# Optimization experiments

Hardware: AMD Instinct MI355X
Metric: run time of the kernel (lower is better)

Reference implementation:

```python
import jax, jax.numpy as jnp
import numpy as np

N_NODES = 100000
N_EDGES = 3200000
D_IN = 128
D_OUT = 128


def setup_inputs() -> dict:
    key = jax.random.key(0)
    k1, k2, k3 = jax.random.split(key, 3)
    x = jax.random.normal(k1, (N_NODES, D_IN), dtype=jnp.float32)
    edge_index = jax.random.randint(k2, (2, N_EDGES), 0, N_NODES, dtype=jnp.int64)
    # Glorot-style init for the GCN linear weight [out, in]
    weight = jax.random.normal(k3, (D_OUT, D_IN), dtype=jnp.float32) * (1.0 / np.sqrt(D_IN))
    bias = jnp.zeros((D_OUT,), dtype=jnp.float32)
    return {"x": x, "edge_index": edge_index, "weight": weight, "bias": bias}


def reference(x, edge_index, weight, bias):
    """LinearEncoder.forward: (GCNConv(x, edge_index), 0).

    GCNConv: out = D^-1/2 (A + I) D^-1/2 (x W^T) + b  (symmetric norm, self-loops).
    """
    n = x.shape[0]
    src = edge_index[0]
    dst = edge_index[1]
    # add self-loops
    loops = jnp.arange(n, dtype=src.dtype)
    src = jnp.concatenate([src, loops])
    dst = jnp.concatenate([dst, loops])
    # degree (in-degree over destination nodes, unit edge weights)
    ones = jnp.ones(src.shape[0], dtype=x.dtype)
    deg = jax.ops.segment_sum(ones, dst, num_segments=n)
    deg_inv_sqrt = jnp.where(deg > 0, jax.lax.rsqrt(deg), 0.0).astype(x.dtype)
    norm = deg_inv_sqrt[src] * deg_inv_sqrt[dst]  # [E+N]
    # dense transform first (as in PyG GCNConv), then sparse aggregation
    h = x @ weight.T  # [N, D_OUT]
    msgs = h[src] * norm[:, None]  # [E+N, D_OUT]
    out = jax.ops.segment_sum(msgs, dst, num_segments=n) + bias
    return (out, 0)
```

## Files before the change

kernel.cpp:

```cpp
#include <hip/hip_runtime.h>
#include <hip/hip_bf16.h>

#define N_NODES 100000
#define N_EDGES 3200000
#define D 128

typedef unsigned short u16;

#define BKT_W 512
#define NBKT 196
#define NSH 8
#define CAPS 2304
#define CAPB (NSH * CAPS)
#define EPB 6400
#define P1B 500
#define EPT 25

#define CY_BLOCKS 6250
#define CW_BLOCKS 8

typedef __attribute__((ext_vector_type(8))) short bf16x8;
typedef __attribute__((ext_vector_type(4))) float f32x4;

__device__ __forceinline__ float bf2f(u16 u) {
    union { unsigned i; float f; } a; a.i = ((unsigned)u) << 16; return a.f;
}
__device__ __forceinline__ u16 f2bf(float f) {
    __hip_bfloat16 b = __float2bfloat16(f);
    return *(u16*)&b;
}

__global__ __launch_bounds__(256) void p1_multisplit(const int* __restrict__ ei,
                                                     int* __restrict__ bcnt,
                                                     unsigned* __restrict__ bbuf) {
    __shared__ unsigned s1[EPB];
    __shared__ unsigned s2[EPB];
    __shared__ int hist[NBKT], lbase[NBKT], cur[NBKT], gbase[NBKT];
    __shared__ int sc[256];
    int t = threadIdx.x, blk = blockIdx.x;
    int sh = blk & (NSH - 1);
    int e0 = blk * EPB;
    if (t < NBKT) hist[t] = 0;
    __syncthreads();

    unsigned char bk[EPT];
#pragma unroll
    for (int k = 0; k < EPT; ++k) {
        int i = k * 256 + t;
        int s = ei[e0 + i];
        int d = ei[N_EDGES + e0 + i];
        unsigned bkt = (unsigned)d >> 9;
        bk[k] = (unsigned char)bkt;
        s1[i] = ((unsigned)s << 9) | ((unsigned)d & 511u);
        atomicAdd(&hist[bkt], 1);
    }
    __syncthreads();

    if (t < NBKT) gbase[t] = atomicAdd(&bcnt[t * NSH + sh], hist[t]);

    sc[t] = (t < NBKT) ? hist[t] : 0;
    __syncthreads();
    for (int o = 1; o < 256; o <<= 1) {
        int u = (t >= o) ? sc[t - o] : 0;
        __syncthreads();
        sc[t] += u;
        __syncthreads();
    }
    if (t < NBKT) { int ex = sc[t] - hist[t]; lbase[t] = ex; cur[t] = ex; }
    __syncthreads();

#pragma unroll
    for (int k = 0; k < EPT; ++k) {
        int i = k * 256 + t;
        int p = atomicAdd(&cur[bk[k]], 1);
        s2[p] = s1[i];
    }
    __syncthreads();

    int wave = t >> 6, lane = t & 63;
    for (int bkt = wave; bkt < NBKT; bkt += 4) {
        int n = hist[bkt], lb = lbase[bkt], gb = gbase[bkt];
        unsigned* dst = bbuf + ((size_t)bkt * NSH + sh) * CAPS;
        for (int j = lane; j < n; j += 64) {
            int p = gb + j;
            if (p < CAPS) dst[p] = s2[lb + j];
        }
    }
}

__global__ __launch_bounds__(256) void p2_localsort(const unsigned* __restrict__ bbuf,
                                                    const int* __restrict__ bcnt,
                                                    int* __restrict__ sorted,
                                                    int* __restrict__ beg_g,
                                                    int* __restrict__ cnt_g,
                                                    float* __restrict__ dinv_g) {
    __shared__ int hist[BKT_W], cur[BKT_W], shcnt[NSH];
    __shared__ int sc[256];
    int b = blockIdx.x, t = threadIdx.x;
    if (t < NSH) { int m = bcnt[b * NSH + t]; shcnt[t] = m > CAPS ? CAPS : m; }
    hist[t] = 0; hist[t + 256] = 0;
    __syncthreads();

    for (int sh = 0; sh < NSH; ++sh) {
        int m = shcnt[sh];
        const unsigned* p = bbuf + ((size_t)b * NSH + sh) * CAPS;
        for (int i = t; i < m; i += 256) atomicAdd(&hist[p[i] & 511u], 1);
    }
    __syncthreads();

    int a0 = hist[2 * t], a1 = hist[2 * t + 1];
    sc[t] = a0 + a1;
    __syncthreads();
    for (int o = 1; o < 256; o <<= 1) {
        int u = (t >= o) ? sc[t - o] : 0;
        __syncthreads();
        sc[t] += u;
        __syncthreads();
    }
    int exp_ = sc[t] - a0 - a1;
    cur[2 * t] = exp_;
    cur[2 * t + 1] = exp_ + a0;
    __syncthreads();

#pragma unroll
    for (int q = 0; q < 2; ++q) {
        int l = t + q * 256;
        int node = b * BKT_W + l;
        if (node < N_NODES) {
            int c = hist[l];
            cnt_g[node] = c;
            beg_g[node] = b * CAPB + cur[l];
            dinv_g[node] = rsqrtf((float)(c + 1));
        }
    }
    __syncthreads();

    int* dst = sorted + (size_t)b * CAPB;
    for (int sh = 0; sh < NSH; ++sh) {
        int m = shcnt[sh];
        const unsigned* p = bbuf + ((size_t)b * NSH + sh) * CAPS;
        for (int i = t; i < m; i += 256) {
            unsigned w = p[i];
            int pp = atomicAdd(&cur[w & 511u], 1);
            dst[pp] = (int)(w >> 9);
        }
    }
}

__global__ __launch_bounds__(256) void convert_yw(const float* __restrict__ x,
                                                  const float* __restrict__ dinv,
                                                  const float* __restrict__ w,
                                                  u16* __restrict__ y,
                                                  u16* __restrict__ wbf) {
    int blk = blockIdx.x;
    if (blk < CY_BLOCKS) {
        int gid = blk * 256 + threadIdx.x;
        size_t e = (size_t)gid * 8;
        float dn = dinv[gid >> 4];
        const float4* xp = (const float4*)(x + e);
        float4 a = xp[0], b = xp[1];
        union { u16 h[8]; uint4 v; } o;
        o.h[0] = f2bf(a.x * dn); o.h[1] = f2bf(a.y * dn);
        o.h[2] = f2bf(a.z * dn); o.h[3] = f2bf(a.w * dn);
        o.h[4] = f2bf(b.x * dn); o.h[5] = f2bf(b.y * dn);
        o.h[6] = f2bf(b.z * dn); o.h[7] = f2bf(b.w * dn);
        ((uint4*)y)[gid] = o.v;
    } else {
        int idx = (blk - CY_BLOCKS) * 256 + threadIdx.x;
        const float4* wp = (const float4*)(w + (size_t)idx * 8);
        float4 a = wp[0], b = wp[1];
        union { u16 h[8]; uint4 v; } o;
        o.h[0] = f2bf(a.x); o.h[1] = f2bf(a.y);
        o.h[2] = f2bf(a.z); o.h[3] = f2bf(a.w);
        o.h[4] = f2bf(b.x); o.h[5] = f2bf(b.y);
        o.h[6] = f2bf(b.z); o.h[7] = f2bf(b.w);
        ((uint4*)wbf)[idx] = o.v;
    }
}

__global__ void aggregate_y_kernel(const u16* __restrict__ y, const float* __restrict__ dinv,
                                   const int* __restrict__ beg_g, const int* __restrict__ cnt_g,
                                   const int* __restrict__ sorted_src,
                                   float* __restrict__ agg) {
    int n = blockIdx.x;
    int t = threadIdx.x;
    float acc = bf2f(y[(size_t)n * D + t]);
    int c = cnt_g[n];
    int beg = beg_g[n];
    int i = 0;
    for (; i + 8 <= c; i += 8) {
        int s[8];
#pragma unroll
        for (int j = 0; j < 8; ++j) s[j] = sorted_src[beg + i + j];
        float v[8];
#pragma unroll
        for (int j = 0; j < 8; ++j) v[j] = bf2f(y[(size_t)s[j] * D + t]);
#pragma unroll
        for (int j = 0; j < 8; ++j) acc += v[j];
    }
    for (; i + 4 <= c; i += 4) {
        int s0 = sorted_src[beg + i];
        int s1 = sorted_src[beg + i + 1];
        int s2 = sorted_src[beg + i + 2];
        int s3 = sorted_src[beg + i + 3];
        float v0 = bf2f(y[(size_t)s0 * D + t]);
        float v1 = bf2f(y[(size_t)s1 * D + t]);
        float v2 = bf2f(y[(size_t)s2 * D + t]);
        float v3 = bf2f(y[(size_t)s3 * D + t]);
        acc += v0; acc += v1; acc += v2; acc += v3;
    }
    for (; i < c; ++i) {
        int s = sorted_src[beg + i];
        acc += bf2f(y[(size_t)s * D + t]);
    }
    agg[(size_t)n * D + t] = acc * dinv[n];
}

__global__ __launch_bounds__(256) void gemm_mfma(const u16* __restrict__ wbf,
                                                 const float* __restrict__ bias,
                                                 float* __restrict__ out) {
    int t = threadIdx.x;
    int wave = t >> 6, lane = t & 63;
    int n0 = blockIdx.x * 64 + wave * 16;
    int lrow = lane & 15;
    int quad = lane >> 4;

    int arow = n0 + lrow;
    const float* ap = out + (size_t)(arow < N_NODES ? arow : 0) * D;
    bf16x8 afrag[4];
#pragma unroll
    for (int kt = 0; kt < 4; ++kt) {
        int k0 = kt * 32 + quad * 8;
        f32x4 x0 = *(const f32x4*)(ap + k0);
        f32x4 x1 = *(const f32x4*)(ap + k0 + 4);
        bf16x8 a;
        a[0] = (short)f2bf(x0.x); a[1] = (short)f2bf(x0.y);
        a[2] = (short)f2bf(x0.z); a[3] = (short)f2bf(x0.w);
        a[4] = (short)f2bf(x1.x); a[5] = (short)f2bf(x1.y);
        a[6] = (short)f2bf(x1.z); a[7] = (short)f2bf(x1.w);
        afrag[kt] = a;
    }

#pragma unroll
    for (int jt = 0; jt < 8; ++jt) {
        int j0 = jt * 16;
        f32x4 acc = {0.f, 0.f, 0.f, 0.f};
#pragma unroll
        for (int kt = 0; kt < 4; ++kt) {
            int k0 = kt * 32 + quad * 8;
            bf16x8 b = *(const bf16x8*)(wbf + (size_t)(j0 + lrow) * D + k0);
            acc = __builtin_amdgcn_mfma_f32_16x16x32_bf16(afrag[kt], b, acc, 0, 0, 0);
        }
        float bb = bias[j0 + lrow];
#pragma unroll
        for (int i = 0; i < 4; ++i) {
            int n = n0 + quad * 4 + i;
            if (n < N_NODES) out[(size_t)n * D + j0 + lrow] = acc[i] + bb;
        }
    }
    if (blockIdx.x == 0 && t == 0) out[(size_t)N_NODES * D] = 0.f;
}

extern "C" void kernel_launch(void* const* d_in, const int* in_sizes, int n_in,
                              void* d_out, int out_size, void* d_ws, size_t ws_size,
                              hipStream_t stream) {
    const float* x = (const float*)d_in[0];
    const int* ei = (const int*)d_in[1];
    const float* w = (const float*)d_in[2];
    const float* bias = (const float*)d_in[3];
    float* out = (float*)d_out;

    char* ws = (char*)d_ws;
    size_t o = 0;
    auto alloc = [&](size_t bytes) -> char* {
        char* p = ws + o;
        o = (o + bytes + 511) & ~(size_t)511;
        return p;
    };
    char* regionA = alloc((size_t)N_NODES * D * 2);
    unsigned* bbuf = (unsigned*)regionA;
    u16* y = (u16*)regionA;
    int* sorted = (int*)alloc((size_t)NBKT * CAPB * 4);
    int* cnt = (int*)alloc((size_t)N_NODES * 4);
    int* beg = (int*)alloc((size_t)N_NODES * 4);
    float* dinv = (float*)alloc((size_t)N_NODES * 4);
    int* bcnt = (int*)alloc((size_t)NBKT * NSH * 4);
    u16* wbf = (u16*)alloc((size_t)D * D * 2);

    hipMemsetAsync(bcnt, 0, (size_t)NBKT * NSH * 4, stream);

    p1_multisplit<<<P1B, 256, 0, stream>>>(ei, bcnt, bbuf);
    p2_localsort<<<NBKT, 256, 0, stream>>>(bbuf, bcnt, sorted, beg, cnt, dinv);
    convert_yw<<<CY_BLOCKS + CW_BLOCKS, 256, 0, stream>>>(x, dinv, w, y, wbf);
    aggregate_y_kernel<<<N_NODES, 128, 0, stream>>>(y, dinv, beg, cnt, sorted, out);
    gemm_mfma<<<(N_NODES + 63) / 64, 256, 0, stream>>>(wbf, bias, out);
}
```

Baseline: 349.2 us.

## Transform before aggregation: fuse x conversion into GEMM, wave-per-node aggregation

Reorders the pipeline so the GEMM reads fp32 x directly, scales rows by dinv and writes bf16 h. The sparse aggregation then sums h and applies dinv and bias in its epilogue. This removes the separate x-to-bf16 conversion pass and the fp32 aggregate write/readback that the final GEMM used to do. The weight conversion moves into extra blocks of the local-sort kernel. Aggregation now gives each node one wave, with each lane reading two packed bf16 values as one 32-bit load and a 16-wide unrolled gather. Aggregating after the transform changes where bf16 rounding happens, which may slightly change numerics.

```diff
diff --git a/kernel.cpp b/kernel.cpp
--- a/kernel.cpp
+++ b/kernel.cpp
@@ -16,7 +16,6 @@
 #define P1B 500
 #define EPT 25
 
-#define CY_BLOCKS 6250
 #define CW_BLOCKS 8
 
 typedef __attribute__((ext_vector_type(8))) short bf16x8;
@@ -24,6 +23,9 @@
 
 __device__ __forceinline__ float bf2f(u16 u) {
     union { unsigned i; float f; } a; a.i = ((unsigned)u) << 16; return a.f;
+}
+__device__ __forceinline__ float asf(unsigned u) {
+    union { unsigned i; float f; } a; a.i = u; return a.f;
 }
 __device__ __forceinline__ u16 f2bf(float f) {
     __hip_bfloat16 b = __float2bfloat16(f);
@@ -93,10 +95,26 @@
                                                     int* __restrict__ sorted,
                                                     int* __restrict__ beg_g,
                                                     int* __restrict__ cnt_g,
-                                                    float* __restrict__ dinv_g) {
+                                                    float* __restrict__ dinv_g,
+                                                    const float* __restrict__ w,
+                                                    u16* __restrict__ wbf) {
     __shared__ int hist[BKT_W], cur[BKT_W], shcnt[NSH];
     __shared__ int sc[256];
     int b = blockIdx.x, t = threadIdx.x;
+
+    if (b >= NBKT) {
+        int idx = (b - NBKT) * 256 + t;
+        const float4* wp = (const float4*)(w + (size_t)idx * 8);
+        float4 a = wp[0], bb = wp[1];
+        union { u16 h[8]; uint4 v; } o;
+        o.h[0] = f2bf(a.x); o.h[1] = f2bf(a.y);
+        o.h[2] = f2bf(a.z); o.h[3] = f2bf(a.w);
+        o.h[4] = f2bf(bb.x); o.h[5] = f2bf(bb.y);
+        o.h[6] = f2bf(bb.z); o.h[7] = f2bf(bb.w);
+        ((uint4*)wbf)[idx] = o.v;
+        return;
+    }
+
     if (t < NSH) { int m = bcnt[b * NSH + t]; shcnt[t] = m > CAPS ? CAPS : m; }
     hist[t] = 0; hist[t + 256] = 0;
     __syncthreads();
@@ -140,85 +158,17 @@
         int m = shcnt[sh];
         const unsigned* p = bbuf + ((size_t)b * NSH + sh) * CAPS;
         for (int i = t; i < m; i += 256) {
-            unsigned w = p[i];
-            int pp = atomicAdd(&cur[w & 511u], 1);
-            dst[pp] = (int)(w >> 9);
-        }
-    }
-}
-
-__global__ __launch_bounds__(256) void convert_yw(const float* __restrict__ x,
-                                                  const float* __restrict__ dinv,
-                                                  const float* __restrict__ w,
-                                                  u16* __restrict__ y,
-                                                  u16* __restrict__ wbf) {
-    int blk = blockIdx.x;
-    if (blk < CY_BLOCKS) {
-        int gid = blk * 256 + threadIdx.x;
-        size_t e = (size_t)gid * 8;
-        float dn = dinv[gid >> 4];
-        const float4* xp = (const float4*)(x + e);
-        float4 a = xp[0], b = xp[1];
-        union { u16 h[8]; uint4 v; } o;
-        o.h[0] = f2bf(a.x * dn); o.h[1] = f2bf(a.y * dn);
-        o.h[2] = f2bf(a.z * dn); o.h[3] = f2bf(a.w * dn);
-        o.h[4] = f2bf(b.x * dn); o.h[5] = f2bf(b.y * dn);
-        o.h[6] = f2bf(b.z * dn); o.h[7] = f2bf(b.w * dn);
-        ((uint4*)y)[gid] = o.v;
-    } else {
-        int idx = (blk - CY_BLOCKS) * 256 + threadIdx.x;
-        const float4* wp = (const float4*)(w + (size_t)idx * 8);
-        float4 a = wp[0], b = wp[1];
-        union { u16 h[8]; uint4 v; } o;
-        o.h[0] = f2bf(a.x); o.h[1] = f2bf(a.y);
-        o.h[2] = f2bf(a.z); o.h[3] = f2bf(a.w);
-        o.h[4] = f2bf(b.x); o.h[5] = f2bf(b.y);
-        o.h[6] = f2bf(b.z); o.h[7] = f2bf(b.w);
-        ((uint4*)wbf)[idx] = o.v;
-    }
-}
-
-__global__ void aggregate_y_kernel(const u16* __restrict__ y, const float* __restrict__ dinv,
-                                   const int* __restrict__ beg_g, const int* __restrict__ cnt_g,
-                                   const int* __restrict__ sorted_src,
-                                   float* __restrict__ agg) {
-    int n = blockIdx.x;
-    int t = threadIdx.x;
-    float acc = bf2f(y[(size_t)n * D + t]);
-    int c = cnt_g[n];
-    int beg = beg_g[n];
-    int i = 0;
-    for (; i + 8 <= c; i += 8) {
-        int s[8];
-#pragma unroll
-        for (int j = 0; j < 8; ++j) s[j] = sorted_src[beg + i + j];
-        float v[8];
-#pragma unroll
-        for (int j = 0; j < 8; ++j) v[j] = bf2f(y[(size_t)s[j] * D + t]);
-#pragma unroll
-        for (int j = 0; j < 8; ++j) acc += v[j];
-    }
-    for (; i + 4 <= c; i += 4) {
-        int s0 = sorted_src[beg + i];
-        int s1 = sorted_src[beg + i + 1];
-        int s2 = sorted_src[beg + i + 2];
-        int s3 = sorted_src[beg + i + 3];
-        float v0 = bf2f(y[(size_t)s0 * D + t]);
-        float v1 = bf2f(y[(size_t)s1 * D + t]);
-        float v2 = bf2f(y[(size_t)s2 * D + t]);
-        float v3 = bf2f(y[(size_t)s3 * D + t]);
-        acc += v0; acc += v1; acc += v2; acc += v3;
-    }
-    for (; i < c; ++i) {
-        int s = sorted_src[beg + i];
-        acc += bf2f(y[(size_t)s * D + t]);
-    }
-    agg[(size_t)n * D + t] = acc * dinv[n];
-}
-
-__global__ __launch_bounds__(256) void gemm_mfma(const u16* __restrict__ wbf,
-                                                 const float* __restrict__ bias,
-                                                 float* __restrict__ out) {
+            unsigned ww = p[i];
+            int pp = atomicAdd(&cur[ww & 511u], 1);
+            dst[pp] = (int)(ww >> 9);
+        }
+    }
+}
+
+__global__ __launch_bounds__(256) void gemm_h(const float* __restrict__ x,
+                                              const u16* __restrict__ wbf,
+                                              const float* __restrict__ dinv,
+                                              u16* __restrict__ h) {
     int t = threadIdx.x;
     int wave = t >> 6, lane = t & 63;
     int n0 = blockIdx.x * 64 + wave * 16;
@@ -226,7 +176,7 @@
     int quad = lane >> 4;
 
     int arow = n0 + lrow;
-    const float* ap = out + (size_t)(arow < N_NODES ? arow : 0) * D;
+    const float* ap = x + (size_t)(arow < N_NODES ? arow : 0) * D;
     bf16x8 afrag[4];
 #pragma unroll
     for (int kt = 0; kt < 4; ++kt) {
@@ -241,6 +191,13 @@
         afrag[kt] = a;
     }
 
+    float dsc[4];
+#pragma unroll
+    for (int i = 0; i < 4; ++i) {
+        int n = n0 + quad * 4 + i;
+        dsc[i] = (n < N_NODES) ? dinv[n] : 0.f;
+    }
+
 #pragma unroll
     for (int jt = 0; jt < 8; ++jt) {
         int j0 = jt * 16;
@@ -251,14 +208,72 @@
             bf16x8 b = *(const bf16x8*)(wbf + (size_t)(j0 + lrow) * D + k0);
             acc = __builtin_amdgcn_mfma_f32_16x16x32_bf16(afrag[kt], b, acc, 0, 0, 0);
         }
-        float bb = bias[j0 + lrow];
 #pragma unroll
         for (int i = 0; i < 4; ++i) {
             int n = n0 + quad * 4 + i;
-            if (n < N_NODES) out[(size_t)n * D + j0 + lrow] = acc[i] + bb;
-        }
-    }
-    if (blockIdx.x == 0 && t == 0) out[(size_t)N_NODES * D] = 0.f;
+            if (n < N_NODES) h[(size_t)n * D + j0 + lrow] = f2bf(acc[i] * dsc[i]);
+        }
+    }
+}
+
+__global__ __launch_bounds__(256) void aggregate_h(const u16* __restrict__ h,
+                                                   const float* __restrict__ dinv,
+                                                   const int* __restrict__ beg_g,
+                                                   const int* __restrict__ cnt_g,
+                                                   const int* __restrict__ sorted_src,
+                                                   const float* __restrict__ bias,
+                                                   float* __restrict__ out) {
+    int w = threadIdx.x >> 6;
+    int l = threadIdx.x & 63;
+    int n = blockIdx.x * 4 + w;
+    const unsigned* h32 = (const unsigned*)h;
+
+    unsigned us = h32[(size_t)n * 64 + l];
+    float acc0 = asf(us << 16);
+    float acc1 = asf(us & 0xffff0000u);
+
+    int c = __builtin_amdgcn_readfirstlane(cnt_g[n]);
+    int beg = __builtin_amdgcn_readfirstlane(beg_g[n]);
+    const int* sp = sorted_src + beg;
+
+    int i = 0;
+    for (; i + 16 <= c; i += 16) {
+        int s[16];
+#pragma unroll
+        for (int j = 0; j < 16; ++j) s[j] = sp[i + j];
+        unsigned u[16];
+#pragma unroll
+        for (int j = 0; j < 16; ++j) u[j] = h32[(size_t)s[j] * 64 + l];
+#pragma unroll
+        for (int j = 0; j < 16; ++j) {
+            acc0 += asf(u[j] << 16);
+            acc1 += asf(u[j] & 0xffff0000u);
+        }
+    }
+    for (; i + 4 <= c; i += 4) {
+        int s0 = sp[i], s1 = sp[i + 1], s2 = sp[i + 2], s3 = sp[i + 3];
+        unsigned u0 = h32[(size_t)s0 * 64 + l];
+        unsigned u1 = h32[(size_t)s1 * 64 + l];
+        unsigned u2 = h32[(size_t)s2 * 64 + l];
+        unsigned u3 = h32[(size_t)s3 * 64 + l];
+        acc0 += asf(u0 << 16); acc1 += asf(u0 & 0xffff0000u);
+        acc0 += asf(u1 << 16); acc1 += asf(u1 & 0xffff0000u);
+        acc0 += asf(u2 << 16); acc1 += asf(u2 & 0xffff0000u);
+        acc0 += asf(u3 << 16); acc1 += asf(u3 & 0xffff0000u);
+    }
+    for (; i < c; ++i) {
+        unsigned u = h32[(size_t)sp[i] * 64 + l];
+        acc0 += asf(u << 16); acc1 += asf(u & 0xffff0000u);
+    }
+
+    float dn = dinv[n];
+    float2 bs = ((const float2*)bias)[l];
+    float2 o;
+    o.x = acc0 * dn + bs.x;
+    o.y = acc1 * dn + bs.y;
+    ((float2*)out)[(size_t)n * 64 + l] = o;
+
+    if (blockIdx.x == 0 && threadIdx.x == 0) out[(size_t)N_NODES * D] = 0.f;
 }
 
 extern "C" void kernel_launch(void* const* d_in, const int* in_sizes, int n_in,
@@ -279,7 +294,7 @@
     };
     char* regionA = alloc((size_t)N_NODES * D * 2);
     unsigned* bbuf = (unsigned*)regionA;
-    u16* y = (u16*)regionA;
+    u16* h = (u16*)regionA;
     int* sorted = (int*)alloc((size_t)NBKT * CAPB * 4);
     int* cnt = (int*)alloc((size_t)N_NODES * 4);
     int* beg = (int*)alloc((size_t)N_NODES * 4);
@@ -290,8 +305,7 @@
     hipMemsetAsync(bcnt, 0, (size_t)NBKT * NSH * 4, stream);
 
     p1_multisplit<<<P1B, 256, 0, stream>>>(ei, bcnt, bbuf);
-    p2_localsort<<<NBKT, 256, 0, stream>>>(bbuf, bcnt, sorted, beg, cnt, dinv);
-    convert_yw<<<CY_BLOCKS + CW_BLOCKS, 256, 0, stream>>>(x, dinv, w, y, wbf);
-    aggregate_y_kernel<<<N_NODES, 128, 0, stream>>>(y, dinv, beg, cnt, sorted, out);
-    gemm_mfma<<<(N_NODES + 63) / 64, 256, 0, stream>>>(wbf, bias, out);
-}
+    p2_localsort<<<NBKT + CW_BLOCKS, 256, 0, stream>>>(bbuf, bcnt, sorted, beg, cnt, dinv, w, wbf);
+    gemm_h<<<(N_NODES + 63) / 64, 256, 0, stream>>>(x, wbf, dinv, h);
+    aggregate_h<<<N_NODES / 4, 256, 0, stream>>>(h, dinv, beg, cnt, sorted, bias, out);
+}
```

New measurement: 322.1 us. -7.7%, faster.
